# Kernel tuning notes

Measured on AMD Instinct MI355X. Metric: run time of the kernel, lower is better.

## Reference

```python
import jax, jax.numpy as jnp
import numpy as np

B, C, T, K = 16, 512, 2048, 64

def setup_inputs() -> dict:
    key = jax.random.key(0)
    k1, k2, k3 = jax.random.split(key, 3)
    v = jax.random.normal(k1, (B, C, T), dtype=jnp.float32)
    # 1x1 Conv1d weights == linear maps over channel dim
    Wk = jax.random.normal(k2, (K, C), dtype=jnp.float32) * 0.02
    bk = jnp.zeros((K,), dtype=jnp.float32)
    Wq = jax.random.normal(k3, (K, C), dtype=jnp.float32) * 0.02
    bq = jnp.zeros((K,), dtype=jnp.float32)
    gamma = jnp.ones((), dtype=jnp.float32)
    return {"v": v, "Wk": Wk, "bk": bk, "Wq": Wq, "bq": bq, "gamma": gamma}

def reference(v, Wk, bk, Wq, bq, gamma):
    # k, q: (B, K, T) via 1x1 conv = channel-wise linear
    k = jnp.einsum('kc,bct->bkt', Wk, v) + bk[None, :, None]
    q = jnp.einsum('kc,bct->bkt', Wq, v) + bq[None, :, None]
    # original: e1[b,d,i,j]=q[b,d,j], e2[b,d,i,j]=k[b,d,i]; sum over d
    # -> s[b,i,j] = sum_d k[b,d,i] * q[b,d,j]  (avoid materializing B,K,T,T)
    s = jnp.einsum('bdi,bdj->bij', k, q)  # (B, T, T)
    a = jax.nn.softmax(s, axis=1)          # softmax over dim=1 (the i axis)
    att = jnp.einsum('bct,btj->bcj', v, a)  # bmm(v, a)
    return v + gamma * att
```

## Files before the change

kernel.cpp:

```cpp
#include <hip/hip_runtime.h>

#define Bc 16
#define Cc 512
#define Tc 2048
#define QT 128
#define KT 64
#define LTS 66

typedef __attribute__((ext_vector_type(8)))  short short8;
typedef __attribute__((ext_vector_type(4)))  float f32x4;
typedef __attribute__((ext_vector_type(16))) float f32x16;
typedef unsigned short u16;

static __device__ __forceinline__ u16 f2bf(float x) {
  unsigned u = __float_as_uint(x);
  u += 0x7FFF + ((u >> 16) & 1);
  return (u16)(u >> 16);
}

static __device__ __forceinline__ unsigned cvt_pk_bf16(float lo, float hi) {
  unsigned r;
  asm("v_cvt_pk_bf16_f32 %0, %1, %2" : "=v"(r) : "v"(lo), "v"(hi));
  return r;
}

static __device__ __forceinline__ void block_sync_lds() {
  __builtin_amdgcn_sched_barrier(0);
  asm volatile("s_waitcnt lgkmcnt(0)" ::: "memory");
  __builtin_amdgcn_s_barrier();
  __builtin_amdgcn_sched_barrier(0);
}

__global__ __launch_bounds__(256) void prep_kernel(
    const float* __restrict__ Wk, const float* __restrict__ Wq,
    const float* __restrict__ bk, const float* __restrict__ bq,
    u16* __restrict__ Wbf, float* __restrict__ bkq)
{
  int idx  = blockIdx.x * 256 + threadIdx.x;
  int base = idx * 4;
  if (base < 128 * Cc) {
    int ch = base >> 9;
    int c  = base & (Cc - 1);
    const float* src = (ch < 64) ? (Wk + (size_t)ch * Cc + c)
                                 : (Wq + (size_t)(ch - 64) * Cc + c);
    f32x4 w = *reinterpret_cast<const f32x4*>(src);
    uint2 o;
    o.x = (unsigned)f2bf(w[0]) | ((unsigned)f2bf(w[1]) << 16);
    o.y = (unsigned)f2bf(w[2]) | ((unsigned)f2bf(w[3]) << 16);
    *reinterpret_cast<uint2*>(Wbf + base) = o;
  }
  if (idx < 128) bkq[idx] = (idx < 64) ? bk[idx] : bq[idx - 64];
}

__global__ __launch_bounds__(256) void kqv_kernel(
    const float* __restrict__ v, const u16* __restrict__ Wbf,
    const float* __restrict__ bkq, u16* __restrict__ kq, u16* __restrict__ vbf)
{
  __shared__ u16 LDSt[2][64][LTS];
  const int b   = blockIdx.y;
  const int t0  = blockIdx.x * 64;
  const int tid = threadIdx.x;
  const int lane = tid & 63;
  const int w    = tid >> 6;
  const int l15  = lane & 15;
  const int lg   = lane >> 4;

  f32x4 acc[8];
  #pragma unroll
  for (int mt = 0; mt < 8; ++mt) acc[mt] = f32x4{0.f, 0.f, 0.f, 0.f};

  const float* vb = v + (size_t)b * Cc * Tc + t0;
  float x[16];
  #pragma unroll
  for (int r = 0; r < 16; ++r) x[r] = vb[(size_t)(w * 16 + r) * Tc + lane];

  int buf = 0;
  for (int c0 = 0; c0 < Cc; c0 += 64, buf ^= 1) {
    #pragma unroll
    for (int r = 0; r < 16; ++r) {
      u16 hb = f2bf(x[r]);
      LDSt[buf][lane][w * 16 + r] = hb;
      vbf[((size_t)b * Cc + c0 + w * 16 + r) * Tc + t0 + lane] = hb;
    }
    block_sync_lds();
    if (c0 + 64 < Cc) {
      #pragma unroll
      for (int r = 0; r < 16; ++r)
        x[r] = vb[(size_t)(c0 + 64 + w * 16 + r) * Tc + lane];
    }
    #pragma unroll
    for (int ks = 0; ks < 2; ++ks) {
      short8 bfrag = *reinterpret_cast<const short8*>(&LDSt[buf][w * 16 + l15][ks * 32 + lg * 8]);
      #pragma unroll
      for (int mt = 0; mt < 8; ++mt) {
        short8 afrag = *reinterpret_cast<const short8*>(
            Wbf + (size_t)(mt * 16 + l15) * Cc + c0 + ks * 32 + lg * 8);
        acc[mt] = __builtin_amdgcn_mfma_f32_16x16x32_bf16(afrag, bfrag, acc[mt], 0, 0, 0);
      }
    }
  }
  const int t = t0 + w * 16 + l15;
  u16* op = kq + ((size_t)b * Tc + t) * 128;
  #pragma unroll
  for (int mt = 0; mt < 8; ++mt) {
    int chb = mt * 16 + lg * 4;
    uint2 o;
    o.x = cvt_pk_bf16(acc[mt][0] + bkq[chb + 0], acc[mt][1] + bkq[chb + 1]);
    o.y = cvt_pk_bf16(acc[mt][2] + bkq[chb + 2], acc[mt][3] + bkq[chb + 3]);
    *reinterpret_cast<uint2*>(op + chb) = o;
  }
}

__global__ __launch_bounds__(512, 2) void attn_kernel(
    const float* __restrict__ v, const u16* __restrict__ vbf,
    const u16* __restrict__ kq, const float* __restrict__ gamma_p,
    float* __restrict__ out)
{
  __shared__ u16 P[2][128 * 64];
  __shared__ __align__(16) float ep_lds[8][32 * 36];
  __shared__ float lsum_lds[QT];
  __shared__ __align__(16) float linv_lds[QT];

  const int L   = blockIdx.x;
  const int lin = (L & 7) * 32 + (L >> 3);
  const int b   = lin >> 4;
  const int j0  = (lin & 15) * QT;
  const int tid = threadIdx.x;
  const int lane = tid & 63;
  const int wid  = tid >> 6;
  const int l15  = lane & 15;
  const int lg   = lane >> 4;
  const int l31  = lane & 31;
  const int kh   = lane >> 5;
  const int c0   = wid * 64;

  short8 qf0, qf1;
  {
    const u16* qp = kq + (size_t)(b * Tc + j0 + wid * 16 + l15) * 128 + 64 + lg * 8;
    qf0 = *reinterpret_cast<const short8*>(qp);
    qf1 = *reinterpret_cast<const short8*>(qp + 32);
  }

  f32x16 O32[2][4];
  #pragma unroll
  for (int a = 0; a < 2; ++a)
    #pragma unroll
    for (int bb = 0; bb < 4; ++bb)
      #pragma unroll
      for (int e = 0; e < 16; ++e) O32[a][bb][e] = 0.f;

  float lsum = 0.f;

  const u16* kbase = kq + (size_t)b * Tc * 128 + lg * 8;
  const u16* vbase = vbf + ((size_t)b * Cc + c0) * Tc;

  short8 kf[4][2];
  short8 vf0[2][2];
  const int vrow = (size_t)0 + l31;

  #pragma unroll
  for (int it = 0; it < 4; ++it) {
    const u16* kp = kbase + (size_t)(it * 16 + l15) * 128;
    kf[it][0] = *reinterpret_cast<const short8*>(kp);
    kf[it][1] = *reinterpret_cast<const short8*>(kp + 32);
  }
  #pragma unroll
  for (int ct = 0; ct < 2; ++ct)
    #pragma unroll
    for (int kk = 0; kk < 2; ++kk)
      vf0[ct][kk] = *reinterpret_cast<const short8*>(
          vbase + (size_t)(ct * 32 + vrow) * Tc + kk * 16 + kh * 8);
  {
    f32x4 sacc[4];
    #pragma unroll
    for (int it = 0; it < 4; ++it) {
      f32x4 s = f32x4{0.f, 0.f, 0.f, 0.f};
      s = __builtin_amdgcn_mfma_f32_16x16x32_bf16(kf[it][0], qf0, s, 0, 0, 0);
      s = __builtin_amdgcn_mfma_f32_16x16x32_bf16(kf[it][1], qf1, s, 0, 0, 0);
      sacc[it] = s;
    }
    u16* prow = &P[0][(wid * 16 + l15) * 64];
    #pragma unroll
    for (int it = 0; it < 4; ++it) {
      float p0 = __expf(sacc[it][0]);
      float p1 = __expf(sacc[it][1]);
      float p2 = __expf(sacc[it][2]);
      float p3 = __expf(sacc[it][3]);
      lsum += (p0 + p1) + (p2 + p3);
      uint2 wv;
      wv.x = cvt_pk_bf16(p0, p1);
      wv.y = cvt_pk_bf16(p2, p3);
      int chk = ((it * 2 + (lg >> 1)) ^ (l15 & 7)) * 8 + (lg & 1) * 4;
      *reinterpret_cast<uint2*>(prow + chk) = wv;
    }
  }
  #pragma unroll
  for (int it = 0; it < 4; ++it) {
    const u16* kp = kbase + (size_t)(KT + it * 16 + l15) * 128;
    kf[it][0] = *reinterpret_cast<const short8*>(kp);
    kf[it][1] = *reinterpret_cast<const short8*>(kp + 32);
  }
  block_sync_lds();

  int pb = 0;
  for (int i0 = 0; i0 < Tc; i0 += KT, pb ^= 1) {
    const bool last = (i0 + KT >= Tc);

    short8 vf1[2][2];
    #pragma unroll
    for (int ct = 0; ct < 2; ++ct)
      #pragma unroll
      for (int kk = 0; kk < 2; ++kk)
        vf1[ct][kk] = *reinterpret_cast<const short8*>(
            vbase + (size_t)(ct * 32 + vrow) * Tc + i0 + 32 + kk * 16 + kh * 8);

    if (!last) {
      f32x4 sacc[4];
      #pragma unroll
      for (int it = 0; it < 4; ++it) {
        f32x4 s = f32x4{0.f, 0.f, 0.f, 0.f};
        s = __builtin_amdgcn_mfma_f32_16x16x32_bf16(kf[it][0], qf0, s, 0, 0, 0);
        s = __builtin_amdgcn_mfma_f32_16x16x32_bf16(kf[it][1], qf1, s, 0, 0, 0);
        sacc[it] = s;
      }
      u16* prow = &P[pb ^ 1][(wid * 16 + l15) * 64];
      #pragma unroll
      for (int it = 0; it < 4; ++it) {
        float p0 = __expf(sacc[it][0]);
        float p1 = __expf(sacc[it][1]);
        float p2 = __expf(sacc[it][2]);
        float p3 = __expf(sacc[it][3]);
        lsum += (p0 + p1) + (p2 + p3);
        uint2 wv;
        wv.x = cvt_pk_bf16(p0, p1);
        wv.y = cvt_pk_bf16(p2, p3);
        int chk = ((it * 2 + (lg >> 1)) ^ (l15 & 7)) * 8 + (lg & 1) * 4;
        *reinterpret_cast<uint2*>(prow + chk) = wv;
      }
    }

    #pragma unroll
    for (int ks = 0; ks < 4; ++ks) {
      short8 pf[4];
      #pragma unroll
      for (int jt = 0; jt < 4; ++jt) {
        int row = jt * 32 + l31;
        int chk = ((ks * 2 + kh) ^ (row & 7)) * 8;
        pf[jt] = *reinterpret_cast<const short8*>(&P[pb][row * 64 + chk]);
      }
      const short8* vsel0 = (ks < 2) ? &vf0[0][ks] : &vf1[0][ks - 2];
      const short8* vsel1 = (ks < 2) ? &vf0[1][ks] : &vf1[1][ks - 2];
      #pragma unroll
      for (int jt = 0; jt < 4; ++jt) {
        O32[0][jt] = __builtin_amdgcn_mfma_f32_32x32x16_bf16(*vsel0, pf[jt], O32[0][jt], 0, 0, 0);
        O32[1][jt] = __builtin_amdgcn_mfma_f32_32x32x16_bf16(*vsel1, pf[jt], O32[1][jt], 0, 0, 0);
      }
    }

    if (!last) {
      if (i0 + 2 * KT < Tc) {
        #pragma unroll
        for (int it = 0; it < 4; ++it) {
          const u16* kp = kbase + (size_t)(i0 + 2 * KT + it * 16 + l15) * 128;
          kf[it][0] = *reinterpret_cast<const short8*>(kp);
          kf[it][1] = *reinterpret_cast<const short8*>(kp + 32);
        }
      }
      #pragma unroll
      for (int ct = 0; ct < 2; ++ct)
        #pragma unroll
        for (int kk = 0; kk < 2; ++kk)
          vf0[ct][kk] = *reinterpret_cast<const short8*>(
              vbase + (size_t)(ct * 32 + vrow) * Tc + (i0 + KT) + kk * 16 + kh * 8);
      block_sync_lds();
    }
  }

  lsum += __shfl_xor(lsum, 16);
  lsum += __shfl_xor(lsum, 32);
  if (lane < 16) lsum_lds[wid * 16 + lane] = lsum;
  __syncthreads();
  const float gamma = *gamma_p;
  if (tid < QT) linv_lds[tid] = gamma / lsum_lds[tid];
  __syncthreads();

  float* ep = ep_lds[wid];
  const int rd_row = lane >> 3;
  const int rd_ch  = lane & 7;
  #pragma unroll
  for (int ct = 0; ct < 2; ++ct) {
    #pragma unroll
    for (int jt = 0; jt < 4; ++jt) {
      #pragma unroll
      for (int reg = 0; reg < 16; ++reg) {
        int cl = (reg & 3) + 8 * (reg >> 2) + 4 * kh;
        ep[cl * 36 + l31] = O32[ct][jt][reg];
      }
      asm volatile("s_waitcnt lgkmcnt(0)" ::: "memory");
      __builtin_amdgcn_sched_barrier(0);
      #pragma unroll
      for (int h = 0; h < 4; ++h) {
        const int row = rd_row + 8 * h;
        f32x4 o4 = *reinterpret_cast<const f32x4*>(&ep[row * 36 + rd_ch * 4]);
        const int jg = jt * 32 + rd_ch * 4;
        f32x4 li = *reinterpret_cast<const f32x4*>(&linv_lds[jg]);
        const int c_glob = c0 + ct * 32 + row;
        const float* vr = v + ((size_t)(b * Cc + c_glob)) * Tc + j0 + jg;
        float* orow = out + ((size_t)(b * Cc + c_glob)) * Tc + j0 + jg;
        f32x4 v4 = *reinterpret_cast<const f32x4*>(vr);
        f32x4 o;
        o[0] = v4[0] + li[0] * o4[0];
        o[1] = v4[1] + li[1] * o4[1];
        o[2] = v4[2] + li[2] * o4[2];
        o[3] = v4[3] + li[3] * o4[3];
        *reinterpret_cast<f32x4*>(orow) = o;
      }
      asm volatile("s_waitcnt lgkmcnt(0)" ::: "memory");
      __builtin_amdgcn_sched_barrier(0);
    }
  }
}

extern "C" void kernel_launch(void* const* d_in, const int* in_sizes, int n_in,
                              void* d_out, int out_size, void* d_ws, size_t ws_size,
                              hipStream_t stream) {
  const float* v  = (const float*)d_in[0];
  const float* Wk = (const float*)d_in[1];
  const float* bk = (const float*)d_in[2];
  const float* Wq = (const float*)d_in[3];
  const float* bq = (const float*)d_in[4];
  const float* gm = (const float*)d_in[5];
  float* out = (float*)d_out;

  char* ws = (char*)d_ws;
  u16*   kqb = (u16*)ws;
  u16*   vbf = (u16*)(ws + 8388608);
  u16*   Wbf = (u16*)(ws + 8388608 + 33554432);
  float* bkq = (float*)(ws + 8388608 + 33554432 + 131072);

  prep_kernel<<<dim3(64), dim3(256), 0, stream>>>(Wk, Wq, bk, bq, Wbf, bkq);
  kqv_kernel<<<dim3(Tc / 64, Bc), dim3(256), 0, stream>>>(v, Wbf, bkq, kqb, vbf);
  attn_kernel<<<dim3((Tc / QT) * Bc), dim3(512), 0, stream>>>(v, vbf, kqb, gm, out);
}
```

Measured before the change: 191.0 us.

## Split waves into two ping-pong groups alternating score and PV phases

The 8 waves are split into two groups of 4. Each group owns 64 query columns and all 512 channels (128 per wave). Within each key tile the groups alternate roles: one computes QK scores, exp and P writes while the other runs the PV MFMAs at raised priority, then they swap after a barrier. This lets exp/VALU work from one group overlap MFMA work from the other. The cost is an extra block barrier per tile, a larger V fragment footprint per wave (4 channel tiles) and more register pressure.

```diff
diff --git a/kernel.cpp b/kernel.cpp
--- a/kernel.cpp
+++ b/kernel.cpp
@@ -5,6 +5,7 @@
 #define Tc 2048
 #define QT 128
 #define KT 64
+#define NT 32
 #define LTS 66
 
 typedef __attribute__((ext_vector_type(8)))  short short8;
@@ -116,7 +117,7 @@
     const u16* __restrict__ kq, const float* __restrict__ gamma_p,
     float* __restrict__ out)
 {
-  __shared__ u16 P[2][128 * 64];
+  __shared__ u16 P[2][2][64 * 64];
   __shared__ __align__(16) float ep_lds[8][32 * 36];
   __shared__ float lsum_lds[QT];
   __shared__ __align__(16) float linv_lds[QT];
@@ -132,20 +133,24 @@
   const int lg   = lane >> 4;
   const int l31  = lane & 31;
   const int kh   = lane >> 5;
-  const int c0   = wid * 64;
+  const int grp  = wid >> 2;
+  const int wg   = wid & 3;
+  const int c0   = wg * 128;
+  const int sj   = grp * 64 + wg * 16;
+  const int prow_base = (wg * 16 + l15) * 64;
 
   short8 qf0, qf1;
   {
-    const u16* qp = kq + (size_t)(b * Tc + j0 + wid * 16 + l15) * 128 + 64 + lg * 8;
+    const u16* qp = kq + (size_t)(b * Tc + j0 + sj + l15) * 128 + 64 + lg * 8;
     qf0 = *reinterpret_cast<const short8*>(qp);
     qf1 = *reinterpret_cast<const short8*>(qp + 32);
   }
 
-  f32x16 O32[2][4];
-  #pragma unroll
-  for (int a = 0; a < 2; ++a)
-    #pragma unroll
-    for (int bb = 0; bb < 4; ++bb)
+  f32x16 O32[4][2];
+  #pragma unroll
+  for (int a = 0; a < 4; ++a)
+    #pragma unroll
+    for (int bb = 0; bb < 2; ++bb)
       #pragma unroll
       for (int e = 0; e < 16; ++e) O32[a][bb][e] = 0.f;
 
@@ -155,8 +160,7 @@
   const u16* vbase = vbf + ((size_t)b * Cc + c0) * Tc;
 
   short8 kf[4][2];
-  short8 vf0[2][2];
-  const int vrow = (size_t)0 + l31;
+  short8 vf01[4][2];
 
   #pragma unroll
   for (int it = 0; it < 4; ++it) {
@@ -165,11 +169,11 @@
     kf[it][1] = *reinterpret_cast<const short8*>(kp + 32);
   }
   #pragma unroll
-  for (int ct = 0; ct < 2; ++ct)
+  for (int ct = 0; ct < 4; ++ct)
     #pragma unroll
     for (int kk = 0; kk < 2; ++kk)
-      vf0[ct][kk] = *reinterpret_cast<const short8*>(
-          vbase + (size_t)(ct * 32 + vrow) * Tc + kk * 16 + kh * 8);
+      vf01[ct][kk] = *reinterpret_cast<const short8*>(
+          vbase + (size_t)(ct * 32 + l31) * Tc + kk * 16 + kh * 8);
   {
     f32x4 sacc[4];
     #pragma unroll
@@ -179,7 +183,7 @@
       s = __builtin_amdgcn_mfma_f32_16x16x32_bf16(kf[it][1], qf1, s, 0, 0, 0);
       sacc[it] = s;
     }
-    u16* prow = &P[0][(wid * 16 + l15) * 64];
+    u16* prow = &P[grp][0][prow_base];
     #pragma unroll
     for (int it = 0; it < 4; ++it) {
       float p0 = __expf(sacc[it][0]);
@@ -202,83 +206,92 @@
   }
   block_sync_lds();
 
-  int pb = 0;
-  for (int i0 = 0; i0 < Tc; i0 += KT, pb ^= 1) {
-    const bool last = (i0 + KT >= Tc);
-
-    short8 vf1[2][2];
-    #pragma unroll
-    for (int ct = 0; ct < 2; ++ct)
-      #pragma unroll
-      for (int kk = 0; kk < 2; ++kk)
-        vf1[ct][kk] = *reinterpret_cast<const short8*>(
-            vbase + (size_t)(ct * 32 + vrow) * Tc + i0 + 32 + kk * 16 + kh * 8);
-
-    if (!last) {
-      f32x4 sacc[4];
-      #pragma unroll
-      for (int it = 0; it < 4; ++it) {
-        f32x4 s = f32x4{0.f, 0.f, 0.f, 0.f};
-        s = __builtin_amdgcn_mfma_f32_16x16x32_bf16(kf[it][0], qf0, s, 0, 0, 0);
-        s = __builtin_amdgcn_mfma_f32_16x16x32_bf16(kf[it][1], qf1, s, 0, 0, 0);
-        sacc[it] = s;
-      }
-      u16* prow = &P[pb ^ 1][(wid * 16 + l15) * 64];
-      #pragma unroll
-      for (int it = 0; it < 4; ++it) {
-        float p0 = __expf(sacc[it][0]);
-        float p1 = __expf(sacc[it][1]);
-        float p2 = __expf(sacc[it][2]);
-        float p3 = __expf(sacc[it][3]);
-        lsum += (p0 + p1) + (p2 + p3);
-        uint2 wv;
-        wv.x = cvt_pk_bf16(p0, p1);
-        wv.y = cvt_pk_bf16(p2, p3);
-        int chk = ((it * 2 + (lg >> 1)) ^ (l15 & 7)) * 8 + (lg & 1) * 4;
-        *reinterpret_cast<uint2*>(prow + chk) = wv;
-      }
-    }
-
-    #pragma unroll
-    for (int ks = 0; ks < 4; ++ks) {
-      short8 pf[4];
-      #pragma unroll
-      for (int jt = 0; jt < 4; ++jt) {
-        int row = jt * 32 + l31;
-        int chk = ((ks * 2 + kh) ^ (row & 7)) * 8;
-        pf[jt] = *reinterpret_cast<const short8*>(&P[pb][row * 64 + chk]);
-      }
-      const short8* vsel0 = (ks < 2) ? &vf0[0][ks] : &vf1[0][ks - 2];
-      const short8* vsel1 = (ks < 2) ? &vf0[1][ks] : &vf1[1][ks - 2];
-      #pragma unroll
-      for (int jt = 0; jt < 4; ++jt) {
-        O32[0][jt] = __builtin_amdgcn_mfma_f32_32x32x16_bf16(*vsel0, pf[jt], O32[0][jt], 0, 0, 0);
-        O32[1][jt] = __builtin_amdgcn_mfma_f32_32x32x16_bf16(*vsel1, pf[jt], O32[1][jt], 0, 0, 0);
-      }
-    }
-
-    if (!last) {
-      if (i0 + 2 * KT < Tc) {
+  for (int i = 0; i < NT; ++i) {
+    const int i0 = i * KT;
+    const int buf = i & 1;
+
+    #pragma unroll
+    for (int slot = 0; slot < 2; ++slot) {
+      const bool produce = (slot == 0) ? (grp == 0) : (grp == 1);
+
+      if (produce) {
+        if (i + 1 < NT) {
+          f32x4 sacc[4];
+          #pragma unroll
+          for (int it = 0; it < 4; ++it) {
+            f32x4 s = f32x4{0.f, 0.f, 0.f, 0.f};
+            s = __builtin_amdgcn_mfma_f32_16x16x32_bf16(kf[it][0], qf0, s, 0, 0, 0);
+            s = __builtin_amdgcn_mfma_f32_16x16x32_bf16(kf[it][1], qf1, s, 0, 0, 0);
+            sacc[it] = s;
+          }
+          if (i + 2 < NT) {
+            #pragma unroll
+            for (int it = 0; it < 4; ++it) {
+              const u16* kp = kbase + (size_t)((i0 + 2 * KT) + it * 16 + l15) * 128;
+              kf[it][0] = *reinterpret_cast<const short8*>(kp);
+              kf[it][1] = *reinterpret_cast<const short8*>(kp + 32);
+            }
+          }
+          u16* prow = &P[grp][buf ^ 1][prow_base];
+          #pragma unroll
+          for (int it = 0; it < 4; ++it) {
+            float p0 = __expf(sacc[it][0]);
+            float p1 = __expf(sacc[it][1]);
+            float p2 = __expf(sacc[it][2]);
+            float p3 = __expf(sacc[it][3]);
+            lsum += (p0 + p1) + (p2 + p3);
+            uint2 wv;
+            wv.x = cvt_pk_bf16(p0, p1);
+            wv.y = cvt_pk_bf16(p2, p3);
+            int chk = ((it * 2 + (lg >> 1)) ^ (l15 & 7)) * 8 + (lg & 1) * 4;
+            *reinterpret_cast<uint2*>(prow + chk) = wv;
+          }
+        }
+      } else {
+        short8 vf23[4][2];
         #pragma unroll
-        for (int it = 0; it < 4; ++it) {
-          const u16* kp = kbase + (size_t)(i0 + 2 * KT + it * 16 + l15) * 128;
-          kf[it][0] = *reinterpret_cast<const short8*>(kp);
-          kf[it][1] = *reinterpret_cast<const short8*>(kp + 32);
+        for (int ct = 0; ct < 4; ++ct)
+          #pragma unroll
+          for (int kk = 0; kk < 2; ++kk)
+            vf23[ct][kk] = *reinterpret_cast<const short8*>(
+                vbase + (size_t)(ct * 32 + l31) * Tc + i0 + 32 + kk * 16 + kh * 8);
+
+        __builtin_amdgcn_s_setprio(1);
+        #pragma unroll
+        for (int ks = 0; ks < 4; ++ks) {
+          short8 pf[2];
+          #pragma unroll
+          for (int jt = 0; jt < 2; ++jt) {
+            int row = jt * 32 + l31;
+            int chk = ((ks * 2 + kh) ^ (row & 7)) * 8;
+            pf[jt] = *reinterpret_cast<const short8*>(&P[grp][buf][row * 64 + chk]);
+          }
+          #pragma unroll
+          for (int ct = 0; ct < 4; ++ct) {
+            const short8 vsel = (ks < 2) ? vf01[ct][ks] : vf23[ct][ks - 2];
+            #pragma unroll
+            for (int jt = 0; jt < 2; ++jt)
+              O32[ct][jt] = __builtin_amdgcn_mfma_f32_32x32x16_bf16(vsel, pf[jt], O32[ct][jt], 0, 0, 0);
+          }
+        }
+        __builtin_amdgcn_s_setprio(0);
+
+        if (i + 1 < NT) {
+          #pragma unroll
+          for (int ct = 0; ct < 4; ++ct)
+            #pragma unroll
+            for (int kk = 0; kk < 2; ++kk)
+              vf01[ct][kk] = *reinterpret_cast<const short8*>(
+                  vbase + (size_t)(ct * 32 + l31) * Tc + (i0 + KT) + kk * 16 + kh * 8);
         }
       }
-      #pragma unroll
-      for (int ct = 0; ct < 2; ++ct)
-        #pragma unroll
-        for (int kk = 0; kk < 2; ++kk)
-          vf0[ct][kk] = *reinterpret_cast<const short8*>(
-              vbase + (size_t)(ct * 32 + vrow) * Tc + (i0 + KT) + kk * 16 + kh * 8);
       block_sync_lds();
     }
   }
 
   lsum += __shfl_xor(lsum, 16);
   lsum += __shfl_xor(lsum, 32);
-  if (lane < 16) lsum_lds[wid * 16 + lane] = lsum;
+  if (lane < 16) lsum_lds[sj + lane] = lsum;
   __syncthreads();
   const float gamma = *gamma_p;
   if (tid < QT) linv_lds[tid] = gamma / lsum_lds[tid];
@@ -288,9 +301,9 @@
   const int rd_row = lane >> 3;
   const int rd_ch  = lane & 7;
   #pragma unroll
-  for (int ct = 0; ct < 2; ++ct) {
-    #pragma unroll
-    for (int jt = 0; jt < 4; ++jt) {
+  for (int ct = 0; ct < 4; ++ct) {
+    #pragma unroll
+    for (int jt = 0; jt < 2; ++jt) {
       #pragma unroll
       for (int reg = 0; reg < 16; ++reg) {
         int cl = (reg & 3) + 8 * (reg >> 2) + 4 * kh;
@@ -302,7 +315,7 @@
       for (int h = 0; h < 4; ++h) {
         const int row = rd_row + 8 * h;
         f32x4 o4 = *reinterpret_cast<const f32x4*>(&ep[row * 36 + rd_ch * 4]);
-        const int jg = jt * 32 + rd_ch * 4;
+        const int jg = grp * 64 + jt * 32 + rd_ch * 4;
         f32x4 li = *reinterpret_cast<const f32x4*>(&linv_lds[jg]);
         const int c_glob = c0 + ct * 32 + row;
         const float* vr = v + ((size_t)(b * Cc + c_glob)) * Tc + j0 + jg;
```

After: 436.2 us. +128.4%, slower.

## Stage K tiles into LDS via async global_load_lds with double buffering

Applied to the files above, without the earlier changes.

Each wave used to load its own copy of the 64x64 K tile from global memory into registers. Now the block loads the tile once into a swizzled LDS buffer with direct global-to-LDS loads, two tiles ahead, and each wave reads its K fragments from LDS. This cuts redundant global and L2 traffic for K and frees registers. The cost is 16KB of extra LDS, which may limit occupancy, and a full __syncthreads in place of the lighter lgkmcnt wait. The correctness of the async load's vmcnt wait before the barrier depends on how the compiler handles it.

```diff
diff --git a/kernel.cpp b/kernel.cpp
--- a/kernel.cpp
+++ b/kernel.cpp
@@ -5,6 +5,7 @@
 #define Tc 2048
 #define QT 128
 #define KT 64
+#define NT 32
 #define LTS 66
 
 typedef __attribute__((ext_vector_type(8)))  short short8;
@@ -22,6 +23,13 @@
   unsigned r;
   asm("v_cvt_pk_bf16_f32 %0, %1, %2" : "=v"(r) : "v"(lo), "v"(hi));
   return r;
+}
+
+static __device__ __forceinline__ void gload_lds16(const u16* gsrc, u16* ldst) {
+  __builtin_amdgcn_global_load_lds(
+      (const __attribute__((address_space(1))) unsigned int*)gsrc,
+      (__attribute__((address_space(3))) unsigned int*)ldst,
+      16, 0, 0);
 }
 
 static __device__ __forceinline__ void block_sync_lds() {
@@ -117,6 +125,7 @@
     float* __restrict__ out)
 {
   __shared__ u16 P[2][128 * 64];
+  __shared__ u16 Klds[2][64 * 64];
   __shared__ __align__(16) float ep_lds[8][32 * 36];
   __shared__ float lsum_lds[QT];
   __shared__ __align__(16) float linv_lds[QT];
@@ -134,6 +143,11 @@
   const int kh   = lane >> 5;
   const int c0   = wid * 64;
 
+  const int sr = wid * 8 + (lane >> 3);
+  const int sc = (lane & 7) ^ ((lane >> 3) & 7);
+  const u16* kqb2 = kq + (size_t)b * Tc * 128;
+  u16* kst_dst = &Klds[0][0] + wid * 8 * 64;
+
   short8 qf0, qf1;
   {
     const u16* qp = kq + (size_t)(b * Tc + j0 + wid * 16 + l15) * 128 + 64 + lg * 8;
@@ -151,26 +165,19 @@
 
   float lsum = 0.f;
 
-  const u16* kbase = kq + (size_t)b * Tc * 128 + lg * 8;
   const u16* vbase = vbf + ((size_t)b * Cc + c0) * Tc;
-
-  short8 kf[4][2];
   short8 vf0[2][2];
-  const int vrow = (size_t)0 + l31;
-
-  #pragma unroll
-  for (int it = 0; it < 4; ++it) {
-    const u16* kp = kbase + (size_t)(it * 16 + l15) * 128;
-    kf[it][0] = *reinterpret_cast<const short8*>(kp);
-    kf[it][1] = *reinterpret_cast<const short8*>(kp + 32);
-  }
-  #pragma unroll
-  for (int ct = 0; ct < 2; ++ct)
-    #pragma unroll
-    for (int kk = 0; kk < 2; ++kk)
-      vf0[ct][kk] = *reinterpret_cast<const short8*>(
-          vbase + (size_t)(ct * 32 + vrow) * Tc + kk * 16 + kh * 8);
+
+  gload_lds16(kqb2 + (size_t)sr * 128 + sc * 8, kst_dst + 0 * 4096);
+  __syncthreads();
   {
+    short8 kf[4][2];
+    #pragma unroll
+    for (int it = 0; it < 4; ++it)
+      #pragma unroll
+      for (int ks = 0; ks < 2; ++ks)
+        kf[it][ks] = *reinterpret_cast<const short8*>(
+            &Klds[0][(it * 16 + l15) * 64 + (((ks * 4 + lg) ^ (l15 & 7)) * 8)]);
     f32x4 sacc[4];
     #pragma unroll
     for (int it = 0; it < 4; ++it) {
@@ -194,17 +201,23 @@
       *reinterpret_cast<uint2*>(prow + chk) = wv;
     }
   }
-  #pragma unroll
-  for (int it = 0; it < 4; ++it) {
-    const u16* kp = kbase + (size_t)(KT + it * 16 + l15) * 128;
-    kf[it][0] = *reinterpret_cast<const short8*>(kp);
-    kf[it][1] = *reinterpret_cast<const short8*>(kp + 32);
-  }
-  block_sync_lds();
+  gload_lds16(kqb2 + (size_t)(KT + sr) * 128 + sc * 8, kst_dst + 1 * 4096);
+  #pragma unroll
+  for (int ct = 0; ct < 2; ++ct)
+    #pragma unroll
+    for (int kk = 0; kk < 2; ++kk)
+      vf0[ct][kk] = *reinterpret_cast<const short8*>(
+          vbase + (size_t)(ct * 32 + l31) * Tc + kk * 16 + kh * 8);
+  __syncthreads();
 
   int pb = 0;
-  for (int i0 = 0; i0 < Tc; i0 += KT, pb ^= 1) {
-    const bool last = (i0 + KT >= Tc);
+  for (int i = 0; i < NT; ++i, pb ^= 1) {
+    const int i0 = i * KT;
+    const bool last = (i + 1 >= NT);
+
+    if (i + 2 < NT)
+      gload_lds16(kqb2 + (size_t)(i0 + 2 * KT + sr) * 128 + sc * 8,
+                  kst_dst + (i & 1) * 4096);
 
     short8 vf1[2][2];
     #pragma unroll
@@ -212,9 +225,16 @@
       #pragma unroll
       for (int kk = 0; kk < 2; ++kk)
         vf1[ct][kk] = *reinterpret_cast<const short8*>(
-            vbase + (size_t)(ct * 32 + vrow) * Tc + i0 + 32 + kk * 16 + kh * 8);
+            vbase + (size_t)(ct * 32 + l31) * Tc + i0 + 32 + kk * 16 + kh * 8);
 
     if (!last) {
+      short8 kf[4][2];
+      #pragma unroll
+      for (int it = 0; it < 4; ++it)
+        #pragma unroll
+        for (int ks = 0; ks < 2; ++ks)
+          kf[it][ks] = *reinterpret_cast<const short8*>(
+              &Klds[(i + 1) & 1][(it * 16 + l15) * 64 + (((ks * 4 + lg) ^ (l15 & 7)) * 8)]);
       f32x4 sacc[4];
       #pragma unroll
       for (int it = 0; it < 4; ++it) {
@@ -258,21 +278,13 @@
     }
 
     if (!last) {
-      if (i0 + 2 * KT < Tc) {
-        #pragma unroll
-        for (int it = 0; it < 4; ++it) {
-          const u16* kp = kbase + (size_t)(i0 + 2 * KT + it * 16 + l15) * 128;
-          kf[it][0] = *reinterpret_cast<const short8*>(kp);
-          kf[it][1] = *reinterpret_cast<const short8*>(kp + 32);
-        }
-      }
       #pragma unroll
       for (int ct = 0; ct < 2; ++ct)
         #pragma unroll
         for (int kk = 0; kk < 2; ++kk)
           vf0[ct][kk] = *reinterpret_cast<const short8*>(
-              vbase + (size_t)(ct * 32 + vrow) * Tc + (i0 + KT) + kk * 16 + kh * 8);
-      block_sync_lds();
+              vbase + (size_t)(ct * 32 + l31) * Tc + (i0 + KT) + kk * 16 + kh * 8);
+      __syncthreads();
     }
   }
 
```

Result: faster. 161.1 us (-15.7%).
